# Kernel optimization log

Measured on AMD Instinct MI355X. Metric: run time of the kernel, lower is better.

The kernel has to match this reference:

```python
import jax, jax.numpy as jnp
import numpy as np

B, L, D = 1, 4096, 1024
H, DH = 16, 64
BASE = 10000.0


def _rope_tables(L, dh, dtype=jnp.float32):
    inv_freq = 1.0 / (BASE ** (jnp.arange(0, dh, 2, dtype=jnp.float32) / dh))
    freqs = jnp.outer(jnp.arange(L, dtype=jnp.float32), inv_freq)  # [L, dh/2]
    return jnp.cos(freqs).astype(dtype), jnp.sin(freqs).astype(dtype)


def _apply_rope(x, cos, sin):
    # x: [B,H,L,dh]; cos/sin: [L,dh/2]
    x1, x2 = x[..., ::2], x[..., 1::2]
    c = cos[None, None]
    s = sin[None, None]
    return jnp.concatenate([x1 * c - x2 * s, x1 * s + x2 * c], axis=-1)


def setup_inputs() -> dict:
    key = jax.random.key(0)
    ks = jax.random.split(key, 5)
    x = jax.random.normal(ks[0], (B, L, D), dtype=jnp.float32)
    mask = jnp.tril(jnp.ones((L, L), dtype=jnp.int32))  # causal 0/1 mask
    sd = 1.0 / np.sqrt(D)
    Wq = jax.random.normal(ks[1], (D, D), dtype=jnp.float32) * sd
    Wk = jax.random.normal(ks[2], (D, D), dtype=jnp.float32) * sd
    Wv = jax.random.normal(ks[3], (D, D), dtype=jnp.float32) * sd
    Wo = jax.random.normal(ks[4], (D, D), dtype=jnp.float32) * sd
    return {"x": x, "mask": mask, "Wq": Wq, "Wk": Wk, "Wv": Wv, "Wo": Wo}


def reference(x, mask, Wq, Wk, Wv, Wo):
    b, l, d = x.shape
    scale = DH ** -0.5
    cos, sin = _rope_tables(l, DH, x.dtype)

    def heads(w):
        return (x @ w.T).reshape(b, l, H, DH).transpose(0, 2, 1, 3)  # [B,H,L,dh]

    q = _apply_rope(heads(Wq), cos, sin)
    k = _apply_rope(heads(Wk), cos, sin)
    v = heads(Wv)

    attn = jnp.einsum('bhqd,bhkd->bhqk', q, k) * scale
    attn = jnp.where(mask[:l, :l] == 0, -jnp.inf, attn)
    attn = jax.nn.softmax(attn, axis=-1)
    out = jnp.einsum('bhqk,bhkd->bhqd', attn, v)
    out = out.transpose(0, 2, 1, 3).reshape(b, l, d)
    return out @ Wo.T
```

## Files before the change

kernel.cpp:

```cpp
#include <hip/hip_runtime.h>
#include <math.h>

#define LSEQ   4096
#define DMODEL 1024
#define NH     16
#define DHEAD  64
#define PSTRIDE 40
#define MASKV  -30000.0f
#define C2SCALE 0.18033688f

typedef __attribute__((ext_vector_type(8))) short  bf16x8;
typedef __attribute__((ext_vector_type(4))) float  floatx4;
typedef unsigned short ushort_t;

#if __has_builtin(__builtin_amdgcn_exp2f)
#define EXP2F __builtin_amdgcn_exp2f
#else
#define EXP2F exp2f
#endif

__device__ __forceinline__ ushort_t f2bf(float x) {
  unsigned u = __builtin_bit_cast(unsigned, x);
  return (ushort_t)((u + 0x7fff + ((u >> 16) & 1)) >> 16);
}
__device__ __forceinline__ unsigned bf16pair(float a, float b) {
  return (unsigned)f2bf(a) | ((unsigned)f2bf(b) << 16);
}
__device__ __forceinline__ unsigned bfpack_trunc(float a, float b) {
  return __builtin_amdgcn_perm(__builtin_bit_cast(unsigned, b),
                               __builtin_bit_cast(unsigned, a), 0x07060302u);
}
__device__ __forceinline__ void gl_lds16(const ushort_t* g, ushort_t* l) {
  __builtin_amdgcn_global_load_lds(
      (const __attribute__((address_space(1))) void*)g,
      (__attribute__((address_space(3))) void*)l, 16, 0, 0);
}

__global__ void prep_fused(const float* __restrict__ x,  const float* __restrict__ wq,
                           const float* __restrict__ wk, const float* __restrict__ wv,
                           const float* __restrict__ wo, ushort_t* __restrict__ dst,
                           float2* __restrict__ rope) {
  if (blockIdx.x >= 8192) {
    const int idx = (blockIdx.x - 8192) * 256 + threadIdx.x;
    const int s = idx >> 5, t = idx & 31;
    const double invf = exp((double)t * -0.28782313662425572);
    const double ang = (double)s * invf;
    rope[idx] = make_float2((float)cos(ang), (float)sin(ang));
    return;
  }
  const size_t e = ((size_t)blockIdx.x * 256 + threadIdx.x) * 4;
  const float* src; size_t off;
  if      (e < (size_t)(4u << 20)) { src = x;  off = e; }
  else if (e < (size_t)(5u << 20)) { src = wq; off = e - (size_t)(4u << 20); }
  else if (e < (size_t)(6u << 20)) { src = wk; off = e - (size_t)(5u << 20); }
  else if (e < (size_t)(7u << 20)) { src = wv; off = e - (size_t)(6u << 20); }
  else                             { src = wo; off = e - (size_t)(7u << 20); }
  const float4 v = *(const float4*)(src + off);
  uint2 p; p.x = bf16pair(v.x, v.y); p.y = bf16pair(v.z, v.w);
  *(uint2*)(dst + e) = p;
}

__global__ __launch_bounds__(512, 2)
void gemm256_qkv(const ushort_t* __restrict__ A, const ushort_t* __restrict__ B,
                 const float2* __restrict__ rope,
                 ushort_t* __restrict__ Qo, ushort_t* __restrict__ Ko,
                 ushort_t* __restrict__ Vo) {
  __shared__ __align__(16) ushort_t smem[69632];
  const int tid  = threadIdx.x;
  const int w    = tid >> 6, lane = tid & 63;
  const int wr   = w >> 2,   wc   = w & 3;
  const int quad = lane >> 4, col = lane & 15;
  const int csw  = col & 7;
  const int bid = blockIdx.x;
  const int nb  = (bid & 7) * 32 + (bid >> 3);
  const int i0 = (nb & 15) * 192;
  const int j0 = (nb >> 4) * 256;

  const ushort_t* Ab = A + (size_t)i0 * DMODEL;
  const ushort_t* Bb = B + (size_t)j0 * DMODEL;

  const int sr8 = lane >> 3;
  const int sc  = ((lane & 7) ^ sr8) * 8;

  floatx4 acc[6][4];
#pragma unroll
  for (int m = 0; m < 6; ++m)
#pragma unroll
    for (int n = 0; n < 4; ++n) acc[m][n] = (floatx4){0.f, 0.f, 0.f, 0.f};

  auto stageA = [&](int kt, int h) {
    ushort_t* dst = smem + (kt % 3) * 12288 + (h * 64 + w * 8) * 64;
    gl_lds16(Ab + (size_t)(h * 64 + w * 8 + sr8) * DMODEL + kt * 64 + sc, dst);
  };
  auto stageB = [&](int kt, int h) {
    ushort_t* dst = smem + 36864 + (kt & 1) * 16384 + (h * 64 + w * 8) * 64;
    gl_lds16(Bb + (size_t)(h * 64 + w * 8 + sr8) * DMODEL + kt * 64 + sc, dst);
  };

  stageA(0, 0); stageA(0, 1); stageA(0, 2);
  stageB(0, 0); stageB(0, 1); stageB(0, 2); stageB(0, 3);
  stageA(1, 0); stageA(1, 1); stageA(1, 2);
  asm volatile("s_waitcnt vmcnt(3)" ::: "memory");
  __builtin_amdgcn_s_barrier();

  for (int t = 0; t < 16; ++t) {
    const ushort_t* As_ = smem + (t % 3) * 12288;
    const ushort_t* Bs_ = smem + 36864 + (t & 1) * 16384;
    const bool preB = (t + 1 < 16);
    const bool preA = (t + 2 < 16);

    bf16x8 af[3], bfr[4];
#pragma unroll
    for (int n = 0; n < 4; ++n)
      bfr[n] = *(const bf16x8*)(Bs_ + (wc * 64 + n * 16 + col) * 64 + ((quad ^ csw) * 8));
#pragma unroll
    for (int m = 0; m < 3; ++m)
      af[m] = *(const bf16x8*)(As_ + (wr * 96 + m * 16 + col) * 64 + ((quad ^ csw) * 8));
    if (preB) { stageB(t + 1, 0); stageB(t + 1, 1); }
    __builtin_amdgcn_s_setprio(1);
#pragma unroll
    for (int m = 0; m < 3; ++m)
#pragma unroll
      for (int n = 0; n < 4; ++n)
        acc[m][n] = __builtin_amdgcn_mfma_f32_16x16x32_bf16(af[m], bfr[n], acc[m][n], 0, 0, 0);
    __builtin_amdgcn_s_setprio(0);
    __builtin_amdgcn_s_barrier();

#pragma unroll
    for (int m = 0; m < 3; ++m)
      af[m] = *(const bf16x8*)(As_ + (wr * 96 + (m + 3) * 16 + col) * 64 + ((quad ^ csw) * 8));
    if (preB) { stageB(t + 1, 2); stageB(t + 1, 3); }
    __builtin_amdgcn_s_setprio(1);
#pragma unroll
    for (int m = 0; m < 3; ++m)
#pragma unroll
      for (int n = 0; n < 4; ++n)
        acc[m + 3][n] = __builtin_amdgcn_mfma_f32_16x16x32_bf16(af[m], bfr[n], acc[m + 3][n], 0, 0, 0);
    __builtin_amdgcn_s_setprio(0);
    __builtin_amdgcn_s_barrier();

#pragma unroll
    for (int n = 0; n < 4; ++n)
      bfr[n] = *(const bf16x8*)(Bs_ + (wc * 64 + n * 16 + col) * 64 + (((4 + quad) ^ csw) * 8));
#pragma unroll
    for (int m = 0; m < 3; ++m)
      af[m] = *(const bf16x8*)(As_ + (wr * 96 + m * 16 + col) * 64 + (((4 + quad) ^ csw) * 8));
    if (preA) { stageA(t + 2, 0); stageA(t + 2, 1); stageA(t + 2, 2); }
    __builtin_amdgcn_s_setprio(1);
#pragma unroll
    for (int m = 0; m < 3; ++m)
#pragma unroll
      for (int n = 0; n < 4; ++n)
        acc[m][n] = __builtin_amdgcn_mfma_f32_16x16x32_bf16(af[m], bfr[n], acc[m][n], 0, 0, 0);
    __builtin_amdgcn_s_setprio(0);
    __builtin_amdgcn_s_barrier();

#pragma unroll
    for (int m = 0; m < 3; ++m)
      af[m] = *(const bf16x8*)(As_ + (wr * 96 + (m + 3) * 16 + col) * 64 + (((4 + quad) ^ csw) * 8));
    __builtin_amdgcn_s_setprio(1);
#pragma unroll
    for (int m = 0; m < 3; ++m)
#pragma unroll
      for (int n = 0; n < 4; ++n)
        acc[m + 3][n] = __builtin_amdgcn_mfma_f32_16x16x32_bf16(af[m], bfr[n], acc[m + 3][n], 0, 0, 0);
    __builtin_amdgcn_s_setprio(0);
    if (preA) asm volatile("s_waitcnt vmcnt(3)" ::: "memory");
    else      asm volatile("s_waitcnt vmcnt(0)" ::: "memory");
    __builtin_amdgcn_s_barrier();
  }

#pragma unroll
  for (int m = 0; m < 6; ++m) {
    const int f0    = i0 + wr * 96 + m * 16 + quad * 4;
    const int which = f0 >> 10;
    const int h     = (f0 >> 6) & 15;
    const int d     = f0 & 63;
    if (which == 2) {
#pragma unroll
      for (int n = 0; n < 4; ++n) {
        const int s = j0 + wc * 64 + n * 16 + col;
#pragma unroll
        for (int r = 0; r < 4; ++r)
          Vo[(size_t)(h * DHEAD + d + r) * LSEQ + s] = f2bf(acc[m][n][r]);
      }
    } else {
      ushort_t* dst = which ? Ko : Qo;
      const float qs = which ? 1.0f : C2SCALE;
      const int t0 = d >> 1;
#pragma unroll
      for (int n = 0; n < 4; ++n) {
        const int s = j0 + wc * 64 + n * 16 + col;
        const float4 cst = *(const float4*)((const float*)rope + ((size_t)s << 6) + t0 * 2);
        ushort_t* ob = dst + ((size_t)h * LSEQ + s) * DHEAD;
        const float x1 = acc[m][n][0], x2 = acc[m][n][1];
        const float y1 = acc[m][n][2], y2 = acc[m][n][3];
        *(unsigned*)(ob + t0)      = bf16pair((x1 * cst.x - x2 * cst.y) * qs,
                                              (y1 * cst.z - y2 * cst.w) * qs);
        *(unsigned*)(ob + t0 + 32) = bf16pair((x1 * cst.y + x2 * cst.x) * qs,
                                              (y1 * cst.w + y2 * cst.z) * qs);
      }
    }
  }
}

template<int MODE>
__global__ __launch_bounds__(256)
void mfma_gemm(const ushort_t* __restrict__ A, const ushort_t* __restrict__ B,
               float* __restrict__ C, const float2* __restrict__ rope,
               ushort_t* __restrict__ Qo, ushort_t* __restrict__ Ko,
               ushort_t* __restrict__ Vo) {
  __shared__ ushort_t As[128 * 64];
  __shared__ ushort_t Bs[128 * 64];
  const int tid  = threadIdx.x;
  const int w    = tid >> 6, lane = tid & 63;
  const int wm   = w >> 1,   wn   = w & 1;
  const int quad = lane >> 4, col = lane & 15;
  const int csw  = col & 7;
  const int bid = blockIdx.y * 32 + blockIdx.x;
  const int nb  = (bid & 7) * 32 + (bid >> 3);
  const int i0 = (nb % 32) * 128;
  const int j0 = (nb / 32) * 128;

  const ushort_t* Ab = A + (size_t)i0 * DMODEL;
  const ushort_t* Bb = B + (size_t)j0 * DMODEL;

  floatx4 acc[4][4];
#pragma unroll
  for (int mt = 0; mt < 4; ++mt)
#pragma unroll
    for (int nt = 0; nt < 4; ++nt) acc[mt][nt] = (floatx4){0.f, 0.f, 0.f, 0.f};

  const int lrow = lane >> 3;
  const int lcol = ((lane & 7) ^ lrow) * 8;

  for (int k0 = 0; k0 < DMODEL; k0 += 64) {
    __syncthreads();
#pragma unroll
    for (int it = 0; it < 4; ++it) {
      const int rb = (it * 4 + w) * 8;
      gl_lds16(Ab + (size_t)(rb + lrow) * DMODEL + k0 + lcol, As + rb * 64);
      gl_lds16(Bb + (size_t)(rb + lrow) * DMODEL + k0 + lcol, Bs + rb * 64);
    }
    __syncthreads();

#pragma unroll
    for (int kk = 0; kk < 64; kk += 32) {
      const int cblk = (kk >> 3) + quad;
      bf16x8 af[4], bfr[4];
#pragma unroll
      for (int mt = 0; mt < 4; ++mt)
        af[mt] = *(const bf16x8*)(As + (wm * 64 + mt * 16 + col) * 64 +
                                  ((cblk ^ csw) * 8));
#pragma unroll
      for (int nt = 0; nt < 4; ++nt)
        bfr[nt] = *(const bf16x8*)(Bs + (wn * 64 + nt * 16 + col) * 64 +
                                   ((cblk ^ csw) * 8));
#pragma unroll
      for (int mt = 0; mt < 4; ++mt)
#pragma unroll
        for (int nt = 0; nt < 4; ++nt)
          acc[mt][nt] = __builtin_amdgcn_mfma_f32_16x16x32_bf16(
              af[mt], bfr[nt], acc[mt][nt], 0, 0, 0);
    }
  }

  if (MODE == 0) {
#pragma unroll
    for (int mt = 0; mt < 4; ++mt) {
      const int i = i0 + wm * 64 + mt * 16 + quad * 4;
#pragma unroll
      for (int nt = 0; nt < 4; ++nt) {
        const int j = j0 + wn * 64 + nt * 16 + col;
#pragma unroll
        for (int r = 0; r < 4; ++r)
          C[(size_t)(i + r) * DMODEL + j] = acc[mt][nt][r];
      }
    }
  } else {
    const int which = i0 >> 10;
#pragma unroll
    for (int mt = 0; mt < 4; ++mt) {
      const int f0 = i0 + wm * 64 + mt * 16 + quad * 4;
      const int h  = (f0 >> 6) & 15;
      const int d  = f0 & 63;
      if (which == 2) {
#pragma unroll
        for (int nt = 0; nt < 4; ++nt) {
          const int s = j0 + wn * 64 + nt * 16 + col;
#pragma unroll
          for (int r = 0; r < 4; ++r)
            Vo[(size_t)(h * DHEAD + d + r) * LSEQ + s] = f2bf(acc[mt][nt][r]);
        }
      } else {
        ushort_t* dst = which ? Ko : Qo;
        const float qs = which ? 1.0f : C2SCALE;
        const int t0 = d >> 1;
#pragma unroll
        for (int nt = 0; nt < 4; ++nt) {
          const int s = j0 + wn * 64 + nt * 16 + col;
          const float4 cst = *(const float4*)((const float*)rope + ((size_t)s << 6) + t0 * 2);
          ushort_t* ob = dst + ((size_t)h * LSEQ + s) * DHEAD;
          const float x1 = acc[mt][nt][0], x2 = acc[mt][nt][1];
          const float y1 = acc[mt][nt][2], y2 = acc[mt][nt][3];
          *(unsigned*)(ob + t0)      = bf16pair((x1 * cst.x - x2 * cst.y) * qs,
                                                (y1 * cst.z - y2 * cst.w) * qs);
          *(unsigned*)(ob + t0 + 32) = bf16pair((x1 * cst.y + x2 * cst.x) * qs,
                                                (y1 * cst.w + y2 * cst.z) * qs);
        }
      }
    }
  }
}

__global__ __launch_bounds__(1024, 4)
void attn_mfma(const ushort_t* __restrict__ Qh, const ushort_t* __restrict__ Kh,
               const ushort_t* __restrict__ Vt, ushort_t* __restrict__ Om) {
  const int h   = blockIdx.x;
  const int g   = blockIdx.y;
  const int tid = threadIdx.x;
  const int w     = tid >> 6;
  const int wl    = w & 3;
  const int half  = (w >> 2) & 1;
  const int ktpar = w >> 3;
  const int wg    = w & 7;
  const int lane = tid & 63;
  const int quad = lane >> 4;
  const int col  = lane & 15;
  const int csw  = col & 7;

  __shared__ __align__(16) char smem[139264];
  ushort_t* Ks   = (ushort_t*)smem;
  ushort_t* Vs   = (ushort_t*)(smem + 49152);
  ushort_t* Ps   = (ushort_t*)(smem + 98304);
  float*    Obuf = (float*)smem;
  __shared__ float lbuf[3][4][2][16];
  ushort_t* psw = Ps + w * (32 * PSTRIDE);

  const int srow = wg * 8 + (lane >> 3);
  const int scol = (((lane & 7) ^ ((lane >> 3) & 7)) * 8);

  for (int pass = 0; pass < 2; ++pass) {
    const int qb      = pass ? (31 - g) : g;
    const int qbase   = qb * 128 + wl * 32;
    const int nkt_max = 2 * qb + 2;
    const int nt2     = nkt_max >> 1;

    bf16x8 qf[2][2];
#pragma unroll
    for (int nq = 0; nq < 2; ++nq)
#pragma unroll
      for (int c = 0; c < 2; ++c)
        qf[nq][c] = *(const bf16x8*)(Qh +
            ((size_t)(h * LSEQ + qbase + nq * 16 + col)) * DHEAD + quad * 8 + c * 32);

    floatx4 ot[4][2];
#pragma unroll
    for (int md = 0; md < 4; ++md)
#pragma unroll
      for (int nq = 0; nq < 2; ++nq) ot[md][nq] = (floatx4){0.f, 0.f, 0.f, 0.f};
    float l_[2] = {0.f, 0.f};

    auto stage = [&](int kt, int b) {
      const int key0 = kt * 64;
      const int boff = (ktpar * 3 + b) * 4096;
      gl_lds16(Kh + ((size_t)(h * LSEQ + key0 + srow)) * DHEAD + scol,
               Ks + boff + wg * 512);
      gl_lds16(Vt + ((size_t)(h * DHEAD + srow)) * LSEQ + key0 + scol,
               Vs + boff + wg * 512);
    };

    stage(ktpar, 0);
    if (nt2 > 1) {
      stage(ktpar + 2, 1);
      asm volatile("s_waitcnt vmcnt(2)" ::: "memory");
    } else {
      asm volatile("s_waitcnt vmcnt(0)" ::: "memory");
    }
    __builtin_amdgcn_s_barrier();
    asm volatile("" ::: "memory");

    int bufn = 0;
    for (int ktt = 0; ktt < nt2; ++ktt) {
      const int kt  = 2 * ktt + ktpar;
      const bool pre = (ktt + 2 < nt2);
      if (pre) {
        const int nb = (bufn >= 1) ? bufn - 1 : 2;
        stage(kt + 4, nb);
      }

      const ushort_t* kb = Ks + (ktpar * 3 + bufn) * 4096;
      const ushort_t* vb = Vs + (ktpar * 3 + bufn) * 4096;

      bf16x8 kf[2][2];
#pragma unroll
      for (int mk = 0; mk < 2; ++mk)
#pragma unroll
        for (int c = 0; c < 2; ++c)
          kf[mk][c] = *(const bf16x8*)(kb + (half * 32 + mk * 16 + col) * 64 +
                                       (((c * 4 + quad) ^ csw) * 8));

      floatx4 st[2][2];
#pragma unroll
      for (int mk = 0; mk < 2; ++mk)
#pragma unroll
        for (int nq = 0; nq < 2; ++nq) st[mk][nq] = (floatx4){0.f, 0.f, 0.f, 0.f};
#pragma unroll
      for (int mk = 0; mk < 2; ++mk)
#pragma unroll
        for (int c = 0; c < 2; ++c)
#pragma unroll
          for (int nq = 0; nq < 2; ++nq)
            st[mk][nq] = __builtin_amdgcn_mfma_f32_16x16x32_bf16(
                kf[mk][c], qf[nq][c], st[mk][nq], 0, 0, 0);

      if (kt >= nkt_max - 2) {
        const int key0 = kt * 64 + half * 32;
#pragma unroll
        for (int mk = 0; mk < 2; ++mk) {
          const int keyb = key0 + mk * 16 + quad * 4;
#pragma unroll
          for (int nq = 0; nq < 2; ++nq) {
            const int q = qbase + nq * 16 + col;
#pragma unroll
            for (int r = 0; r < 4; ++r)
              if (keyb + r > q) st[mk][nq][r] = MASKV;
          }
        }
      }

#pragma unroll
      for (int mk = 0; mk < 2; ++mk)
#pragma unroll
        for (int nq = 0; nq < 2; ++nq) {
#pragma unroll
          for (int r = 0; r < 4; ++r) st[mk][nq][r] = EXP2F(st[mk][nq][r]);
          l_[nq] += (st[mk][nq][0] + st[mk][nq][1]) + (st[mk][nq][2] + st[mk][nq][3]);
        }

#pragma unroll
      for (int mk = 0; mk < 2; ++mk)
#pragma unroll
        for (int nq = 0; nq < 2; ++nq) {
          uint2 pk;
          pk.x = bfpack_trunc(st[mk][nq][0], st[mk][nq][1]);
          pk.y = bfpack_trunc(st[mk][nq][2], st[mk][nq][3]);
          *(uint2*)(psw + (nq * 16 + col) * PSTRIDE + mk * 16 + quad * 4) = pk;
        }
      bf16x8 pf[2];
#pragma unroll
      for (int nq = 0; nq < 2; ++nq)
        pf[nq] = *(const bf16x8*)(psw + (nq * 16 + col) * PSTRIDE + quad * 8);

      bf16x8 vf[4];
#pragma unroll
      for (int md = 0; md < 4; ++md)
        vf[md] = *(const bf16x8*)(vb + (md * 16 + col) * 64 +
                                  (((half * 4 + quad) ^ csw) * 8));
#pragma unroll
      for (int md = 0; md < 4; ++md)
#pragma unroll
        for (int nq = 0; nq < 2; ++nq)
          ot[md][nq] = __builtin_amdgcn_mfma_f32_16x16x32_bf16(
              vf[md], pf[nq], ot[md][nq], 0, 0, 0);

      if (pre) asm volatile("s_waitcnt vmcnt(2)" ::: "memory");
      else     asm volatile("s_waitcnt vmcnt(0)" ::: "memory");
      __builtin_amdgcn_s_barrier();
      asm volatile("" ::: "memory");
      bufn = (bufn == 2) ? 0 : bufn + 1;
    }

    float lr[2];
#pragma unroll
    for (int nq = 0; nq < 2; ++nq) {
      float ls = l_[nq];
      ls += __shfl_xor(ls, 16);
      ls += __shfl_xor(ls, 32);
      lr[nq] = ls;
    }

    const int di = ((half << 1) | ktpar) - 1;
    if (di >= 0) {
#pragma unroll
      for (int nq = 0; nq < 2; ++nq) {
        if (quad == 0) lbuf[di][wl][nq][col] = lr[nq];
#pragma unroll
        for (int md = 0; md < 4; ++md)
          *(float4*)(Obuf + di * 8704 + ((wl * 2 + nq) * 16 + col) * 68 + md * 16 + quad * 4) =
              (float4){ot[md][nq][0], ot[md][nq][1], ot[md][nq][2], ot[md][nq][3]};
      }
    }
    __syncthreads();

    if (di < 0) {
#pragma unroll
      for (int nq = 0; nq < 2; ++nq) {
        const float inv = 1.0f / (lr[nq] + lbuf[0][wl][nq][col] +
                                  lbuf[1][wl][nq][col] + lbuf[2][wl][nq][col]);
        const int q = qbase + nq * 16 + col;
#pragma unroll
        for (int md = 0; md < 4; ++md) {
          const int ob_off = ((wl * 2 + nq) * 16 + col) * 68 + md * 16 + quad * 4;
          const float4 o0 = *(const float4*)(Obuf + ob_off);
          const float4 o1 = *(const float4*)(Obuf + 8704 + ob_off);
          const float4 o2 = *(const float4*)(Obuf + 17408 + ob_off);
          uint2 pk;
          pk.x = bf16pair((ot[md][nq][0] + o0.x + o1.x + o2.x) * inv,
                          (ot[md][nq][1] + o0.y + o1.y + o2.y) * inv);
          pk.y = bf16pair((ot[md][nq][2] + o0.z + o1.z + o2.z) * inv,
                          (ot[md][nq][3] + o0.w + o1.w + o2.w) * inv);
          *(uint2*)(Om + (size_t)q * DMODEL + h * DHEAD + md * 16 + quad * 4) = pk;
        }
      }
    }
    __syncthreads();
  }
}

extern "C" void kernel_launch(void* const* d_in, const int* in_sizes, int n_in,
                              void* d_out, int out_size, void* d_ws, size_t ws_size,
                              hipStream_t stream) {
  const float* x  = (const float*)d_in[0];
  const float* Wq = (const float*)d_in[2];
  const float* Wk = (const float*)d_in[3];
  const float* Wv = (const float*)d_in[4];
  const float* Wo = (const float*)d_in[5];
  float* out = (float*)d_out;

  const size_t M1 = (size_t)1 << 20;
  ushort_t* xb  = (ushort_t*)d_ws;
  ushort_t* Wb  = xb  + 4 * M1;
  ushort_t* wob = Wb  + 3 * M1;
  ushort_t* Qh  = wob + 1 * M1;
  ushort_t* Kh  = Qh  + 4 * M1;
  ushort_t* Vt  = Kh  + 4 * M1;
  ushort_t* Om  = Vt  + 4 * M1;
  float2*   rope = (float2*)(Om + 4 * M1);

  prep_fused<<<8704, 256, 0, stream>>>(x, Wq, Wk, Wv, Wo, xb, rope);
  gemm256_qkv<<<256, 512, 0, stream>>>(Wb, xb, rope, Qh, Kh, Vt);
  attn_mfma<<<dim3(NH, 16), 1024, 0, stream>>>(Qh, Kh, Vt, Om);
  mfma_gemm<0><<<dim3(32, 8), 256, 0, stream>>>(
      Om, wob, out, nullptr, nullptr, nullptr, nullptr);
}
```

Before: 235.2 us.

## Split attention into smaller 64-query blocks without paired-pass or key-tile parity split

Attention blocks now handle 64 queries each with 512 threads, and the grid grows from 16x16 to 16x64 blocks. This replaces the earlier scheme in which each 1024-thread block processed two paired query tiles of 128 rows and split the key tiles by parity across wave groups. Shared memory per block drops from 136KB to about 58KB, so more blocks can fit per CU and the 4-way cross-wave reduction shrinks to a 2-way one. The cost is that each block reuses Q and K/V less and loads K/V tiles more times overall. Causal load balancing now relies on launching the largest query blocks first instead of pairing short and long tiles inside one block.

```diff
diff --git a/kernel.cpp b/kernel.cpp
--- a/kernel.cpp
+++ b/kernel.cpp
@@ -313,208 +313,160 @@
   }
 }
 
-__global__ __launch_bounds__(1024, 4)
+__global__ __launch_bounds__(512, 4)
 void attn_mfma(const ushort_t* __restrict__ Qh, const ushort_t* __restrict__ Kh,
                const ushort_t* __restrict__ Vt, ushort_t* __restrict__ Om) {
   const int h   = blockIdx.x;
-  const int g   = blockIdx.y;
+  const int qb  = 63 - blockIdx.y;
   const int tid = threadIdx.x;
-  const int w     = tid >> 6;
-  const int wl    = w & 3;
-  const int half  = (w >> 2) & 1;
-  const int ktpar = w >> 3;
-  const int wg    = w & 7;
+  const int w    = tid >> 6;
+  const int wl   = w & 3;
+  const int half = w >> 2;
   const int lane = tid & 63;
   const int quad = lane >> 4;
   const int col  = lane & 15;
   const int csw  = col & 7;
 
-  __shared__ __align__(16) char smem[139264];
+  __shared__ __align__(16) char smem[59392];
   ushort_t* Ks   = (ushort_t*)smem;
-  ushort_t* Vs   = (ushort_t*)(smem + 49152);
-  ushort_t* Ps   = (ushort_t*)(smem + 98304);
+  ushort_t* Vs   = (ushort_t*)(smem + 24576);
+  ushort_t* Ps   = (ushort_t*)(smem + 49152);
   float*    Obuf = (float*)smem;
-  __shared__ float lbuf[3][4][2][16];
-  ushort_t* psw = Ps + w * (32 * PSTRIDE);
-
-  const int srow = wg * 8 + (lane >> 3);
+  __shared__ float lbuf[4][16];
+  ushort_t* psw = Ps + w * (16 * PSTRIDE);
+
+  const int qbase = qb * 64 + wl * 16;
+  const int nkt   = qb + 1;
+
+  const int srow = w * 8 + (lane >> 3);
   const int scol = (((lane & 7) ^ ((lane >> 3) & 7)) * 8);
 
-  for (int pass = 0; pass < 2; ++pass) {
-    const int qb      = pass ? (31 - g) : g;
-    const int qbase   = qb * 128 + wl * 32;
-    const int nkt_max = 2 * qb + 2;
-    const int nt2     = nkt_max >> 1;
-
-    bf16x8 qf[2][2];
-#pragma unroll
-    for (int nq = 0; nq < 2; ++nq)
+  bf16x8 qf[2];
+#pragma unroll
+  for (int c = 0; c < 2; ++c)
+    qf[c] = *(const bf16x8*)(Qh +
+        ((size_t)(h * LSEQ + qbase + col)) * DHEAD + quad * 8 + c * 32);
+
+  floatx4 ot[4];
+#pragma unroll
+  for (int md = 0; md < 4; ++md) ot[md] = (floatx4){0.f, 0.f, 0.f, 0.f};
+  float l_ = 0.f;
+
+  auto stage = [&](int kt, int b) {
+    const int key0 = kt * 64;
+    gl_lds16(Kh + ((size_t)(h * LSEQ + key0 + srow)) * DHEAD + scol,
+             Ks + b * 4096 + w * 512);
+    gl_lds16(Vt + ((size_t)(h * DHEAD + srow)) * LSEQ + key0 + scol,
+             Vs + b * 4096 + w * 512);
+  };
+
+  stage(0, 0);
+  if (nkt > 1) {
+    stage(1, 1);
+    asm volatile("s_waitcnt vmcnt(2)" ::: "memory");
+  } else {
+    asm volatile("s_waitcnt vmcnt(0)" ::: "memory");
+  }
+  __builtin_amdgcn_s_barrier();
+  asm volatile("" ::: "memory");
+
+  int bufn = 0;
+  for (int kt = 0; kt < nkt; ++kt) {
+    const bool pre = (kt + 2 < nkt);
+    if (pre) {
+      const int nb = (bufn >= 1) ? bufn - 1 : 2;
+      stage(kt + 2, nb);
+    }
+
+    const ushort_t* kb = Ks + bufn * 4096;
+    const ushort_t* vb = Vs + bufn * 4096;
+
+    bf16x8 kf[2][2];
+#pragma unroll
+    for (int mk = 0; mk < 2; ++mk)
 #pragma unroll
       for (int c = 0; c < 2; ++c)
-        qf[nq][c] = *(const bf16x8*)(Qh +
-            ((size_t)(h * LSEQ + qbase + nq * 16 + col)) * DHEAD + quad * 8 + c * 32);
-
-    floatx4 ot[4][2];
+        kf[mk][c] = *(const bf16x8*)(kb + (half * 32 + mk * 16 + col) * 64 +
+                                     (((c * 4 + quad) ^ csw) * 8));
+
+    floatx4 st[2];
+#pragma unroll
+    for (int mk = 0; mk < 2; ++mk) st[mk] = (floatx4){0.f, 0.f, 0.f, 0.f};
+#pragma unroll
+    for (int mk = 0; mk < 2; ++mk)
+#pragma unroll
+      for (int c = 0; c < 2; ++c)
+        st[mk] = __builtin_amdgcn_mfma_f32_16x16x32_bf16(
+            kf[mk][c], qf[c], st[mk], 0, 0, 0);
+
+    if (kt == nkt - 1) {
+      const int key0 = kt * 64 + half * 32;
+      const int q = qbase + col;
+#pragma unroll
+      for (int mk = 0; mk < 2; ++mk) {
+        const int keyb = key0 + mk * 16 + quad * 4;
+#pragma unroll
+        for (int r = 0; r < 4; ++r)
+          if (keyb + r > q) st[mk][r] = MASKV;
+      }
+    }
+
+#pragma unroll
+    for (int mk = 0; mk < 2; ++mk) {
+#pragma unroll
+      for (int r = 0; r < 4; ++r) st[mk][r] = EXP2F(st[mk][r]);
+      l_ += (st[mk][0] + st[mk][1]) + (st[mk][2] + st[mk][3]);
+    }
+
+#pragma unroll
+    for (int mk = 0; mk < 2; ++mk) {
+      uint2 pk;
+      pk.x = bfpack_trunc(st[mk][0], st[mk][1]);
+      pk.y = bfpack_trunc(st[mk][2], st[mk][3]);
+      *(uint2*)(psw + col * PSTRIDE + mk * 16 + quad * 4) = pk;
+    }
+    bf16x8 pf = *(const bf16x8*)(psw + col * PSTRIDE + quad * 8);
+
+    bf16x8 vf[4];
 #pragma unroll
     for (int md = 0; md < 4; ++md)
-#pragma unroll
-      for (int nq = 0; nq < 2; ++nq) ot[md][nq] = (floatx4){0.f, 0.f, 0.f, 0.f};
-    float l_[2] = {0.f, 0.f};
-
-    auto stage = [&](int kt, int b) {
-      const int key0 = kt * 64;
-      const int boff = (ktpar * 3 + b) * 4096;
-      gl_lds16(Kh + ((size_t)(h * LSEQ + key0 + srow)) * DHEAD + scol,
-               Ks + boff + wg * 512);
-      gl_lds16(Vt + ((size_t)(h * DHEAD + srow)) * LSEQ + key0 + scol,
-               Vs + boff + wg * 512);
-    };
-
-    stage(ktpar, 0);
-    if (nt2 > 1) {
-      stage(ktpar + 2, 1);
-      asm volatile("s_waitcnt vmcnt(2)" ::: "memory");
-    } else {
-      asm volatile("s_waitcnt vmcnt(0)" ::: "memory");
-    }
+      vf[md] = *(const bf16x8*)(vb + (md * 16 + col) * 64 +
+                                (((half * 4 + quad) ^ csw) * 8));
+#pragma unroll
+    for (int md = 0; md < 4; ++md)
+      ot[md] = __builtin_amdgcn_mfma_f32_16x16x32_bf16(vf[md], pf, ot[md], 0, 0, 0);
+
+    if (pre) asm volatile("s_waitcnt vmcnt(2)" ::: "memory");
+    else     asm volatile("s_waitcnt vmcnt(0)" ::: "memory");
     __builtin_amdgcn_s_barrier();
     asm volatile("" ::: "memory");
-
-    int bufn = 0;
-    for (int ktt = 0; ktt < nt2; ++ktt) {
-      const int kt  = 2 * ktt + ktpar;
-      const bool pre = (ktt + 2 < nt2);
-      if (pre) {
-        const int nb = (bufn >= 1) ? bufn - 1 : 2;
-        stage(kt + 4, nb);
-      }
-
-      const ushort_t* kb = Ks + (ktpar * 3 + bufn) * 4096;
-      const ushort_t* vb = Vs + (ktpar * 3 + bufn) * 4096;
-
-      bf16x8 kf[2][2];
-#pragma unroll
-      for (int mk = 0; mk < 2; ++mk)
-#pragma unroll
-        for (int c = 0; c < 2; ++c)
-          kf[mk][c] = *(const bf16x8*)(kb + (half * 32 + mk * 16 + col) * 64 +
-                                       (((c * 4 + quad) ^ csw) * 8));
-
-      floatx4 st[2][2];
-#pragma unroll
-      for (int mk = 0; mk < 2; ++mk)
-#pragma unroll
-        for (int nq = 0; nq < 2; ++nq) st[mk][nq] = (floatx4){0.f, 0.f, 0.f, 0.f};
-#pragma unroll
-      for (int mk = 0; mk < 2; ++mk)
-#pragma unroll
-        for (int c = 0; c < 2; ++c)
-#pragma unroll
-          for (int nq = 0; nq < 2; ++nq)
-            st[mk][nq] = __builtin_amdgcn_mfma_f32_16x16x32_bf16(
-                kf[mk][c], qf[nq][c], st[mk][nq], 0, 0, 0);
-
-      if (kt >= nkt_max - 2) {
-        const int key0 = kt * 64 + half * 32;
-#pragma unroll
-        for (int mk = 0; mk < 2; ++mk) {
-          const int keyb = key0 + mk * 16 + quad * 4;
-#pragma unroll
-          for (int nq = 0; nq < 2; ++nq) {
-            const int q = qbase + nq * 16 + col;
-#pragma unroll
-            for (int r = 0; r < 4; ++r)
-              if (keyb + r > q) st[mk][nq][r] = MASKV;
-          }
-        }
-      }
-
-#pragma unroll
-      for (int mk = 0; mk < 2; ++mk)
-#pragma unroll
-        for (int nq = 0; nq < 2; ++nq) {
-#pragma unroll
-          for (int r = 0; r < 4; ++r) st[mk][nq][r] = EXP2F(st[mk][nq][r]);
-          l_[nq] += (st[mk][nq][0] + st[mk][nq][1]) + (st[mk][nq][2] + st[mk][nq][3]);
-        }
-
-#pragma unroll
-      for (int mk = 0; mk < 2; ++mk)
-#pragma unroll
-        for (int nq = 0; nq < 2; ++nq) {
-          uint2 pk;
-          pk.x = bfpack_trunc(st[mk][nq][0], st[mk][nq][1]);
-          pk.y = bfpack_trunc(st[mk][nq][2], st[mk][nq][3]);
-          *(uint2*)(psw + (nq * 16 + col) * PSTRIDE + mk * 16 + quad * 4) = pk;
-        }
-      bf16x8 pf[2];
-#pragma unroll
-      for (int nq = 0; nq < 2; ++nq)
-        pf[nq] = *(const bf16x8*)(psw + (nq * 16 + col) * PSTRIDE + quad * 8);
-
-      bf16x8 vf[4];
-#pragma unroll
-      for (int md = 0; md < 4; ++md)
-        vf[md] = *(const bf16x8*)(vb + (md * 16 + col) * 64 +
-                                  (((half * 4 + quad) ^ csw) * 8));
-#pragma unroll
-      for (int md = 0; md < 4; ++md)
-#pragma unroll
-        for (int nq = 0; nq < 2; ++nq)
-          ot[md][nq] = __builtin_amdgcn_mfma_f32_16x16x32_bf16(
-              vf[md], pf[nq], ot[md][nq], 0, 0, 0);
-
-      if (pre) asm volatile("s_waitcnt vmcnt(2)" ::: "memory");
-      else     asm volatile("s_waitcnt vmcnt(0)" ::: "memory");
-      __builtin_amdgcn_s_barrier();
-      asm volatile("" ::: "memory");
-      bufn = (bufn == 2) ? 0 : bufn + 1;
-    }
-
-    float lr[2];
-#pragma unroll
-    for (int nq = 0; nq < 2; ++nq) {
-      float ls = l_[nq];
-      ls += __shfl_xor(ls, 16);
-      ls += __shfl_xor(ls, 32);
-      lr[nq] = ls;
-    }
-
-    const int di = ((half << 1) | ktpar) - 1;
-    if (di >= 0) {
-#pragma unroll
-      for (int nq = 0; nq < 2; ++nq) {
-        if (quad == 0) lbuf[di][wl][nq][col] = lr[nq];
-#pragma unroll
-        for (int md = 0; md < 4; ++md)
-          *(float4*)(Obuf + di * 8704 + ((wl * 2 + nq) * 16 + col) * 68 + md * 16 + quad * 4) =
-              (float4){ot[md][nq][0], ot[md][nq][1], ot[md][nq][2], ot[md][nq][3]};
-      }
-    }
-    __syncthreads();
-
-    if (di < 0) {
-#pragma unroll
-      for (int nq = 0; nq < 2; ++nq) {
-        const float inv = 1.0f / (lr[nq] + lbuf[0][wl][nq][col] +
-                                  lbuf[1][wl][nq][col] + lbuf[2][wl][nq][col]);
-        const int q = qbase + nq * 16 + col;
-#pragma unroll
-        for (int md = 0; md < 4; ++md) {
-          const int ob_off = ((wl * 2 + nq) * 16 + col) * 68 + md * 16 + quad * 4;
-          const float4 o0 = *(const float4*)(Obuf + ob_off);
-          const float4 o1 = *(const float4*)(Obuf + 8704 + ob_off);
-          const float4 o2 = *(const float4*)(Obuf + 17408 + ob_off);
-          uint2 pk;
-          pk.x = bf16pair((ot[md][nq][0] + o0.x + o1.x + o2.x) * inv,
-                          (ot[md][nq][1] + o0.y + o1.y + o2.y) * inv);
-          pk.y = bf16pair((ot[md][nq][2] + o0.z + o1.z + o2.z) * inv,
-                          (ot[md][nq][3] + o0.w + o1.w + o2.w) * inv);
-          *(uint2*)(Om + (size_t)q * DMODEL + h * DHEAD + md * 16 + quad * 4) = pk;
-        }
-      }
-    }
-    __syncthreads();
+    bufn = (bufn == 2) ? 0 : bufn + 1;
+  }
+
+  float lr = l_;
+  lr += __shfl_xor(lr, 16);
+  lr += __shfl_xor(lr, 32);
+
+  if (half == 1) {
+    if (quad == 0) lbuf[wl][col] = lr;
+#pragma unroll
+    for (int md = 0; md < 4; ++md)
+      *(float4*)(Obuf + (wl * 16 + col) * 68 + md * 16 + quad * 4) =
+          (float4){ot[md][0], ot[md][1], ot[md][2], ot[md][3]};
+  }
+  __syncthreads();
+
+  if (half == 0) {
+    const float inv = 1.0f / (lr + lbuf[wl][col]);
+    const int q = qbase + col;
+#pragma unroll
+    for (int md = 0; md < 4; ++md) {
+      const float4 ob = *(const float4*)(Obuf + (wl * 16 + col) * 68 + md * 16 + quad * 4);
+      uint2 pk;
+      pk.x = bf16pair((ot[md][0] + ob.x) * inv, (ot[md][1] + ob.y) * inv);
+      pk.y = bf16pair((ot[md][2] + ob.z) * inv, (ot[md][3] + ob.w) * inv);
+      *(uint2*)(Om + (size_t)q * DMODEL + h * DHEAD + md * 16 + quad * 4) = pk;
+    }
   }
 }
 
@@ -540,7 +492,7 @@
 
   prep_fused<<<8704, 256, 0, stream>>>(x, Wq, Wk, Wv, Wo, xb, rope);
   gemm256_qkv<<<256, 512, 0, stream>>>(Wb, xb, rope, Qh, Kh, Vt);
-  attn_mfma<<<dim3(NH, 16), 1024, 0, stream>>>(Qh, Kh, Vt, Om);
+  attn_mfma<<<dim3(NH, 64), 512, 0, stream>>>(Qh, Kh, Vt, Om);
   mfma_gemm<0><<<dim3(32, 8), 256, 0, stream>>>(
       Om, wob, out, nullptr, nullptr, nullptr, nullptr);
 }
```

After: 240.6 us. 1.02x slower.
